# Optimization experiments

Hardware: AMD Instinct MI355X
Metric: run time of the kernel (lower is better)

The kernel has to match this reference:

```python
import jax, jax.numpy as jnp
import numpy as np

B, N, E = 8, 4096, 131072
NODE_DIM, HIDDEN = 64, 128


def _mlp2(x, W1, b1, W2, b2):
    # Linear -> SiLU -> Linear
    return jax.nn.silu(x @ W1 + b1) @ W2 + b2


def setup_inputs() -> dict:
    key = jax.random.key(0)
    ks = jax.random.split(key, 10)
    inp = {
        "node_features": jax.random.normal(ks[0], (B, N, NODE_DIM), jnp.float32),
        "coords": jax.random.normal(ks[1], (B, N, 3), jnp.float32),
        "edge_index": jax.random.randint(ks[2], (2, E), 0, N, jnp.int32),
        # message_net: in = 2*node_dim + 1 = 129
        "Wm1": jax.random.normal(ks[3], (2 * NODE_DIM + 1, HIDDEN), jnp.float32) * 0.05,
        "bm1": jnp.zeros((HIDDEN,), jnp.float32),
        "Wm2": jax.random.normal(ks[4], (HIDDEN, HIDDEN), jnp.float32) * 0.05,
        "bm2": jnp.zeros((HIDDEN,), jnp.float32),
        # node_update: in = node_dim + hidden = 192
        "Wn1": jax.random.normal(ks[5], (NODE_DIM + HIDDEN, HIDDEN), jnp.float32) * 0.05,
        "bn1": jnp.zeros((HIDDEN,), jnp.float32),
        "Wn2": jax.random.normal(ks[6], (HIDDEN, NODE_DIM), jnp.float32) * 0.05,
        "bn2": jnp.zeros((NODE_DIM,), jnp.float32),
        # coord_update: hidden -> hidden -> 1
        "Wc1": jax.random.normal(ks[7], (HIDDEN, HIDDEN), jnp.float32) * 0.05,
        "bc1": jnp.zeros((HIDDEN,), jnp.float32),
        "Wc2": jax.random.normal(ks[8], (HIDDEN, 1), jnp.float32) * 0.05,
        "bc2": jnp.zeros((1,), jnp.float32),
    }
    return inp


def reference(node_features, coords, edge_index, Wm1, bm1, Wm2, bm2,
              Wn1, bn1, Wn2, bn2, Wc1, bc1, Wc2, bc2):
    src, dst = edge_index[0], edge_index[1]
    # Gather per-edge geometry: [B, E, 3]
    edge_vec = coords[:, dst, :] - coords[:, src, :]
    edge_dist = jnp.linalg.norm(edge_vec, axis=-1, keepdims=True)  # [B,E,1]
    edge_vec_n = edge_vec / (edge_dist + 1e-8)
    # Gather node features per edge and build message input: [B, E, 2*D+1]
    msg_in = jnp.concatenate(
        [node_features[:, src, :], node_features[:, dst, :], edge_dist], axis=-1)
    messages = _mlp2(msg_in, Wm1, bm1, Wm2, bm2)  # [B, E, H]
    # Scatter-add messages into destination nodes: [B, N, H]
    agg = jnp.zeros((node_features.shape[0], node_features.shape[1], messages.shape[-1]),
                    dtype=messages.dtype).at[:, dst, :].add(messages)
    # Residual node update
    nf_new = node_features + _mlp2(
        jnp.concatenate([node_features, agg], axis=-1), Wn1, bn1, Wn2, bn2)
    # Equivariant coordinate update
    coord_w = _mlp2(messages, Wc1, bc1, Wc2, bc2)  # [B, E, 1]
    coord_delta = jnp.zeros_like(coords).at[:, dst, :].add(coord_w * edge_vec_n)
    coords_new = coords + coord_delta
    return nf_new, coords_new
```

## Files before the change

### kernel.cpp

```cpp
#include <hip/hip_runtime.h>
#include <hip/hip_bf16.h>

#define B_ 8
#define N_ 4096
#define E_ 131072
#define D_ 64
#define H_ 128

#define EDGE_BLOCKS 256
#define ETILE 128
#define TILES_TOTAL ((B_ * E_) / ETILE)
#define TILES_PER_BLOCK (TILES_TOTAL / EDGE_BLOCKS)

typedef unsigned int u32;
typedef short bf16x8 __attribute__((ext_vector_type(8)));
typedef float f32x4 __attribute__((ext_vector_type(4)));

__device__ __forceinline__ unsigned short f2bf(float f) {
  u32 x = __float_as_uint(f);
  x += 0x7fffu + ((x >> 16) & 1u);
  return (unsigned short)(x >> 16);
}
__device__ __forceinline__ float bf2f(unsigned short v) {
  return __uint_as_float(((u32)v) << 16);
}
__device__ __forceinline__ float silu_f(float x) { return x / (1.0f + __expf(-x)); }

__device__ __forceinline__ int swz(int row, int col) {
  return row * 128 + (col ^ ((row & 7) << 3));
}

__device__ __forceinline__ void gemm128(const unsigned short* in,
                                        const unsigned short* wT,
                                        int rA, int rB, int k0l, f32x4 acc[2][2]) {
#pragma unroll
  for (int ks = 0; ks < 4; ++ks) {
    const int k = ks * 32 + k0l;
    bf16x8 a0 = *(const bf16x8*)&in[swz(rA, k)];
    bf16x8 a1 = *(const bf16x8*)&in[swz(rA + 16, k)];
    bf16x8 b0 = *(const bf16x8*)&wT[swz(rB, k)];
    bf16x8 b1 = *(const bf16x8*)&wT[swz(rB + 16, k)];
    acc[0][0] = __builtin_amdgcn_mfma_f32_16x16x32_bf16(a0, b0, acc[0][0], 0, 0, 0);
    acc[0][1] = __builtin_amdgcn_mfma_f32_16x16x32_bf16(a0, b1, acc[0][1], 0, 0, 0);
    acc[1][0] = __builtin_amdgcn_mfma_f32_16x16x32_bf16(a1, b0, acc[1][0], 0, 0, 0);
    acc[1][1] = __builtin_amdgcn_mfma_f32_16x16x32_bf16(a1, b1, acc[1][1], 0, 0, 0);
  }
}

__global__ void nf2bf_k(const float* __restrict__ nf, unsigned short* __restrict__ nf16) {
  const int i = blockIdx.x * 256 + threadIdx.x;
  float4 v = ((const float4*)nf)[i];
  u32 p0 = (u32)f2bf(v.x) | ((u32)f2bf(v.y) << 16);
  u32 p1 = (u32)f2bf(v.z) | ((u32)f2bf(v.w) << 16);
  ((uint2*)nf16)[i] = make_uint2(p0, p1);
}

__global__ void hist_k(const int* __restrict__ ei, int* __restrict__ hist) {
  const int e = blockIdx.x * 256 + threadIdx.x;
  atomicAdd(&hist[ei[E_ + e]], 1);
}

__global__ __launch_bounds__(1024) void scan4096(int* __restrict__ h) {
  __shared__ int wsums[16];
  const int tid = threadIdx.x;
  const int lane = tid & 63, wv = tid >> 6;
  int4 v = ((int4*)h)[tid];
  const int s = v.x + v.y + v.z + v.w;
  int incl = s;
#pragma unroll
  for (int off = 1; off < 64; off <<= 1) {
    int u = __shfl_up(incl, off);
    if (lane >= off) incl += u;
  }
  if (lane == 63) wsums[wv] = incl;
  __syncthreads();
  if (wv == 0) {
    int ws = (lane < 16) ? wsums[lane] : 0;
#pragma unroll
    for (int off = 1; off < 16; off <<= 1) {
      int u = __shfl_up(ws, off);
      if (lane >= off) ws += u;
    }
    if (lane < 16) wsums[lane] = ws;
  }
  __syncthreads();
  int base = (wv ? wsums[wv - 1] : 0) + (incl - s);
  int4 o;
  o.x = base; o.y = base + v.x; o.z = o.y + v.y; o.w = o.z + v.z;
  ((int4*)h)[tid] = o;
}

__global__ void scatter_k(const int* __restrict__ ei, int* __restrict__ offs,
                          int* __restrict__ src_s, int* __restrict__ dst_s) {
  const int e = blockIdx.x * 256 + threadIdx.x;
  const int d = ei[E_ + e];
  const int p = atomicAdd(&offs[d], 1);
  src_s[p] = ei[e];
  dst_s[p] = d;
}

__global__ __launch_bounds__(1024, 4) void egnn_edge_mfma(
    const unsigned short* __restrict__ nf16, const float* __restrict__ coords,
    const int* __restrict__ src_s, const int* __restrict__ dst_s,
    const float* __restrict__ Wm1, const float* __restrict__ bm1,
    const float* __restrict__ Wm2, const float* __restrict__ bm2,
    const float* __restrict__ Wc1, const float* __restrict__ bc1,
    const float* __restrict__ Wc2, const float* __restrict__ bc2,
    float* __restrict__ agg, float* __restrict__ cdelta)
{
  __shared__ unsigned short sW1[128 * 128];
  __shared__ unsigned short sW2[128 * 128];
  __shared__ unsigned short sW3[128 * 128];
  __shared__ unsigned short buf[ETILE * 128];
  __shared__ float4 sgeo[2][ETILE];
  __shared__ int sdst[2][ETILE];
  __shared__ float swpart[4][ETILE];

  const int tid = threadIdx.x;
  for (int i = tid; i < 128 * 128; i += 1024) {
    const int k = i >> 7, n = i & 127;
    const int d = swz(n, k);
    sW1[d] = f2bf(Wm1[i]);
    sW2[d] = f2bf(Wm2[i]);
    sW3[d] = f2bf(Wc1[i]);
  }

  const int lane = tid & 63;
  const int w = tid >> 6;
  const int l15 = lane & 15;
  const int l4 = lane >> 4;
  const int k0l = l4 * 8;
  const int rowbase = (w >> 2) * 32;
  const int colbase = (w & 3) * 32;
  const int rA = rowbase + l15;
  const int rB = colbase + l15;
  const int n0 = colbase + l15;
  const int n1 = n0 + 16;

  const float bb1_0 = bm1[n0], bb1_1 = bm1[n1];
  const float bb2_0 = bm2[n0], bb2_1 = bm2[n1];
  const float bb3_0 = bc1[n0], bb3_1 = bc1[n1];
  const float wc2_0 = Wc2[n0], wc2_1 = Wc2[n1];
  const float wr_0 = Wm1[128 * 128 + n0], wr_1 = Wm1[128 * 128 + n1];
  const float bc2v = bc2[0];

  const int m_t = tid >> 3;
  const int q_t = tid & 7;

  const int myblk = (blockIdx.x & 7) * (EDGE_BLOCKS / 8) + (blockIdx.x >> 3);
  const int b = myblk >> 5;
  const int gbase = (myblk & 31) * TILES_PER_BLOCK;

  __syncthreads();

  for (int t = 0; t < TILES_PER_BLOCK; ++t) {
    const int p = t & 1;
    const int ebase = (gbase + t) * ETILE;

    if (tid < ETILE) {
      const int e = ebase + tid;
      const int s = src_s[e];
      const int d = dst_s[e];
      sdst[p][tid] = d;
      const float* cs = coords + (size_t)(b * N_ + s) * 3;
      const float* cd = coords + (size_t)(b * N_ + d) * 3;
      const float d0 = cd[0] - cs[0], d1 = cd[1] - cs[1], d2 = cd[2] - cs[2];
      const float dist = sqrtf(fmaf(d0, d0, fmaf(d1, d1, d2 * d2)));
      sgeo[p][tid] = make_float4(d0, d1, d2, dist);
    }
    {
      const int e = ebase + m_t;
      const int s = src_s[e];
      const int d = dst_s[e];
      const uint4* ps = (const uint4*)(nf16 + (size_t)(b * N_ + s) * 64);
      const uint4* pd = (const uint4*)(nf16 + (size_t)(b * N_ + d) * 64);
      uint4 vs = ps[q_t];
      uint4 vd = pd[q_t];
      *(uint4*)&buf[swz(m_t, q_t * 8)] = vs;
      *(uint4*)&buf[swz(m_t, 64 + q_t * 8)] = vd;
    }
    __syncthreads();

    f32x4 acc[2][2];
    {
      f32x4 z = {0.f, 0.f, 0.f, 0.f};
      acc[0][0] = z; acc[0][1] = z; acc[1][0] = z; acc[1][1] = z;
    }
    gemm128(buf, sW1, rA, rB, k0l, acc);
    float hv[2][2][4];
#pragma unroll
    for (int i = 0; i < 2; ++i)
#pragma unroll
      for (int r = 0; r < 4; ++r) {
        const int m = rowbase + 16 * i + l4 * 4 + r;
        const float dist = sgeo[p][m].w;
        hv[i][0][r] = silu_f(acc[i][0][r] + bb1_0 + dist * wr_0);
        hv[i][1][r] = silu_f(acc[i][1][r] + bb1_1 + dist * wr_1);
      }
    __syncthreads();
#pragma unroll
    for (int i = 0; i < 2; ++i)
#pragma unroll
      for (int r = 0; r < 4; ++r) {
        const int m = rowbase + 16 * i + l4 * 4 + r;
        buf[swz(m, n0)] = f2bf(hv[i][0][r]);
        buf[swz(m, n1)] = f2bf(hv[i][1][r]);
      }
    __syncthreads();

    {
      f32x4 z = {0.f, 0.f, 0.f, 0.f};
      acc[0][0] = z; acc[0][1] = z; acc[1][0] = z; acc[1][1] = z;
    }
    gemm128(buf, sW2, rA, rB, k0l, acc);
    float mv0[2][4], mv1[2][4];
#pragma unroll
    for (int i = 0; i < 2; ++i)
#pragma unroll
      for (int r = 0; r < 4; ++r) {
        mv0[i][r] = acc[i][0][r] + bb2_0;
        mv1[i][r] = acc[i][1][r] + bb2_1;
      }
    __syncthreads();
#pragma unroll
    for (int i = 0; i < 2; ++i)
#pragma unroll
      for (int r = 0; r < 4; ++r) {
        const int m = rowbase + 16 * i + l4 * 4 + r;
        buf[swz(m, n0)] = f2bf(mv0[i][r]);
        buf[swz(m, n1)] = f2bf(mv1[i][r]);
      }
    __syncthreads();

    {
      f32x4 z = {0.f, 0.f, 0.f, 0.f};
      acc[0][0] = z; acc[0][1] = z; acc[1][0] = z; acc[1][1] = z;
    }
    gemm128(buf, sW3, rA, rB, k0l, acc);
#pragma unroll
    for (int i = 0; i < 2; ++i)
#pragma unroll
      for (int r = 0; r < 4; ++r) {
        float pw = silu_f(acc[i][0][r] + bb3_0) * wc2_0 +
                   silu_f(acc[i][1][r] + bb3_1) * wc2_1;
        pw += __shfl_xor(pw, 1);
        pw += __shfl_xor(pw, 2);
        pw += __shfl_xor(pw, 4);
        pw += __shfl_xor(pw, 8);
        if (l15 == 0) swpart[w & 3][rowbase + 16 * i + l4 * 4 + r] = pw;
      }

    {
      const int c = tid & 127;
      int r = (tid >> 7) * 16;
      int cur = sdst[p][r];
      float accs = 0.f;
#pragma unroll 4
      for (int k = 0; k < 16; ++k, ++r) {
        const int d2 = sdst[p][r];
        if (d2 != cur) {
          unsafeAtomicAdd(agg + ((size_t)(b * N_ + cur)) * H_ + c, accs);
          accs = 0.f;
          cur = d2;
        }
        accs += bf2f(buf[swz(r, c)]);
      }
      unsafeAtomicAdd(agg + ((size_t)(b * N_ + cur)) * H_ + c, accs);
    }
    __syncthreads();

    if (tid < ETILE) {
      float wc = bc2v;
#pragma unroll
      for (int cg = 0; cg < 4; ++cg) wc += swpart[cg][tid];
      const float4 g = sgeo[p][tid];
      const float inv = 1.0f / (g.w + 1e-8f);
      float vx = wc * g.x * inv, vy = wc * g.y * inv, vz = wc * g.z * inv;
      const int myd = sdst[p][tid];
      int flg = (lane == 0) ? 1 : (sdst[p][tid - 1] != myd);
#pragma unroll
      for (int off = 1; off < 64; off <<= 1) {
        float ux = __shfl_up(vx, off);
        float uy = __shfl_up(vy, off);
        float uz = __shfl_up(vz, off);
        int uf = __shfl_up(flg, off);
        if (lane >= off) {
          if (!flg) { vx += ux; vy += uy; vz += uz; }
          flg |= uf;
        }
      }
      const bool tail = (lane == 63) || (sdst[p][tid + 1] != myd);
      if (tail) {
        float* bp = cdelta + ((size_t)(b * N_ + myd)) * 3;
        unsafeAtomicAdd(bp + 0, vx);
        unsafeAtomicAdd(bp + 1, vy);
        unsafeAtomicAdd(bp + 2, vz);
      }
    }
  }
}

__device__ __forceinline__ float bfbits(u32 x) { return __uint_as_float(x); }

__global__ __launch_bounds__(512, 2) void egnn_node(
    const float* __restrict__ nf, const float* __restrict__ coords,
    const float* __restrict__ agg, const float* __restrict__ cdelta,
    const float* __restrict__ Wn1, const float* __restrict__ bn1,
    const float* __restrict__ Wn2, const float* __restrict__ bn2,
    float* __restrict__ out_nf, float* __restrict__ out_c)
{
  __shared__ unsigned short sWn1[192 * H_];
  __shared__ unsigned short sWn2[H_ * D_];
  __shared__ float sb[192];
  __shared__ float swork[8][328];

  const int tid = threadIdx.x;
  for (int i = tid; i < 192 * H_; i += 512) sWn1[i] = f2bf(Wn1[i]);
  for (int i = tid; i < H_ * D_; i += 512) sWn2[i] = f2bf(Wn2[i]);
  if (tid < 128) sb[tid] = bn1[tid];
  if (tid >= 128 && tid < 192) sb[tid] = bn2[tid - 128];
  __syncthreads();

  const int wave = tid >> 6;
  const int lane = tid & 63;
  float* W = swork[wave];

  const int total = B_ * N_;
  const int stride = gridDim.x * 8;

  for (int task = blockIdx.x * 8 + wave; task < total; task += stride) {
    const float* nfp = nf + (size_t)task * D_;
    const float* ap = agg + (size_t)task * H_;
    W[lane] = nfp[lane];
    W[64 + lane] = ap[lane];
    W[128 + lane] = ap[64 + lane];
    __syncthreads();

    {
      const unsigned short* wp = sWn1 + 2 * lane;
      float a0 = 0.f, a1 = 0.f, a2 = 0.f, a3 = 0.f;
#pragma unroll 8
      for (int k = 0; k < 192; k += 2) {
        float2 x = *(const float2*)&W[k];
        u32 p0 = *(const u32*)(wp + k * H_);
        u32 p1 = *(const u32*)(wp + (k + 1) * H_);
        a0 = fmaf(x.x, bfbits(p0 << 16), a0);
        a1 = fmaf(x.x, bfbits(p0 & 0xffff0000u), a1);
        a2 = fmaf(x.y, bfbits(p1 << 16), a2);
        a3 = fmaf(x.y, bfbits(p1 & 0xffff0000u), a3);
      }
      float h0 = silu_f(a0 + a2 + sb[2 * lane]);
      float h1 = silu_f(a1 + a3 + sb[2 * lane + 1]);
      ((float2*)(W + 192))[lane] = make_float2(h0, h1);
    }
    __syncthreads();

    {
      float a0 = 0.f, a1 = 0.f, a2 = 0.f, a3 = 0.f;
#pragma unroll 8
      for (int k = 0; k < 128; k += 4) {
        float2 xa = *(const float2*)&W[192 + k];
        float2 xb = *(const float2*)&W[192 + k + 2];
        a0 = fmaf(xa.x, bfbits(((u32)sWn2[(k + 0) * D_ + lane]) << 16), a0);
        a1 = fmaf(xa.y, bfbits(((u32)sWn2[(k + 1) * D_ + lane]) << 16), a1);
        a2 = fmaf(xb.x, bfbits(((u32)sWn2[(k + 2) * D_ + lane]) << 16), a2);
        a3 = fmaf(xb.y, bfbits(((u32)sWn2[(k + 3) * D_ + lane]) << 16), a3);
      }
      out_nf[(size_t)task * D_ + lane] =
          nfp[lane] + (a0 + a1 + a2 + a3) + sb[128 + lane];
      if (lane < 3) {
        out_c[(size_t)task * 3 + lane] =
            coords[(size_t)task * 3 + lane] + cdelta[(size_t)task * 3 + lane];
      }
    }
    __syncthreads();
  }
}

extern "C" void kernel_launch(void* const* d_in, const int* in_sizes, int n_in,
                              void* d_out, int out_size, void* d_ws, size_t ws_size,
                              hipStream_t stream) {
  const float* nf     = (const float*)d_in[0];
  const float* coords = (const float*)d_in[1];
  const int*   ei     = (const int*)d_in[2];
  const float* Wm1 = (const float*)d_in[3];
  const float* bm1 = (const float*)d_in[4];
  const float* Wm2 = (const float*)d_in[5];
  const float* bm2 = (const float*)d_in[6];
  const float* Wn1 = (const float*)d_in[7];
  const float* bn1 = (const float*)d_in[8];
  const float* Wn2 = (const float*)d_in[9];
  const float* bn2 = (const float*)d_in[10];
  const float* Wc1 = (const float*)d_in[11];
  const float* bc1 = (const float*)d_in[12];
  const float* Wc2 = (const float*)d_in[13];
  const float* bc2 = (const float*)d_in[14];

  float* agg    = (float*)d_ws;
  float* cdelta = agg + (size_t)B_ * N_ * H_;
  int*   hist   = (int*)(cdelta + (size_t)B_ * N_ * 3);
  int*   src_s  = hist + 4096;
  int*   dst_s  = src_s + E_;

  float* out_nf = (float*)d_out;
  float* out_c  = out_nf + (size_t)B_ * N_ * D_;

  unsigned short* nf16 = (unsigned short*)d_out;

  const size_t zero_bytes =
      ((size_t)B_ * N_ * H_ + (size_t)B_ * N_ * 3 + 4096) * sizeof(float);
  hipMemsetAsync(d_ws, 0, zero_bytes, stream);

  nf2bf_k<<<(B_ * N_ * D_ / 4) / 256, 256, 0, stream>>>(nf, nf16);
  hist_k<<<E_ / 256, 256, 0, stream>>>(ei, hist);
  scan4096<<<1, 1024, 0, stream>>>(hist);
  scatter_k<<<E_ / 256, 256, 0, stream>>>(ei, hist, src_s, dst_s);

  egnn_edge_mfma<<<EDGE_BLOCKS, 1024, 0, stream>>>(
      nf16, coords, src_s, dst_s, Wm1, bm1, Wm2, bm2, Wc1, bc1, Wc2, bc2,
      agg, cdelta);
  egnn_node<<<512, 512, 0, stream>>>(nf, coords, agg, cdelta,
                                     Wn1, bn1, Wn2, bn2, out_nf, out_c);
}
```

Before: 456.0 us.

## Double edge tile, register-resident Wc1 fragments, prefetch next tile gathers

Doubles the edge tile to 256 rows so each wave computes a 64x32 output block, reusing each B fragment across four A fragments. The third weight matrix is held in registers instead of LDS, which frees shared memory for the larger buffer. Node-feature gathers and geometry for the next tile are prefetched into registers and the spare sgeo/sdst buffer while the current tile computes. Float-to-bf16 conversion now uses the packed hardware instruction. The cost is much higher register pressure under launch_bounds(1024,4), which risks spills or lower occupancy.

```diff
diff --git a/kernel.cpp b/kernel.cpp
--- a/kernel.cpp
+++ b/kernel.cpp
@@ -8,7 +8,7 @@
 #define H_ 128
 
 #define EDGE_BLOCKS 256
-#define ETILE 128
+#define ETILE 256
 #define TILES_TOTAL ((B_ * E_) / ETILE)
 #define TILES_PER_BLOCK (TILES_TOTAL / EDGE_BLOCKS)
 
@@ -24,34 +24,24 @@
 __device__ __forceinline__ float bf2f(unsigned short v) {
   return __uint_as_float(((u32)v) << 16);
 }
+__device__ __forceinline__ u32 cvt_pk_bf16(float lo, float hi) {
+  u32 r;
+  asm("v_cvt_pk_bf16_f32 %0, %1, %2" : "=v"(r) : "v"(lo), "v"(hi));
+  return r;
+}
 __device__ __forceinline__ float silu_f(float x) { return x / (1.0f + __expf(-x)); }
 
 __device__ __forceinline__ int swz(int row, int col) {
   return row * 128 + (col ^ ((row & 7) << 3));
 }
 
-__device__ __forceinline__ void gemm128(const unsigned short* in,
-                                        const unsigned short* wT,
-                                        int rA, int rB, int k0l, f32x4 acc[2][2]) {
-#pragma unroll
-  for (int ks = 0; ks < 4; ++ks) {
-    const int k = ks * 32 + k0l;
-    bf16x8 a0 = *(const bf16x8*)&in[swz(rA, k)];
-    bf16x8 a1 = *(const bf16x8*)&in[swz(rA + 16, k)];
-    bf16x8 b0 = *(const bf16x8*)&wT[swz(rB, k)];
-    bf16x8 b1 = *(const bf16x8*)&wT[swz(rB + 16, k)];
-    acc[0][0] = __builtin_amdgcn_mfma_f32_16x16x32_bf16(a0, b0, acc[0][0], 0, 0, 0);
-    acc[0][1] = __builtin_amdgcn_mfma_f32_16x16x32_bf16(a0, b1, acc[0][1], 0, 0, 0);
-    acc[1][0] = __builtin_amdgcn_mfma_f32_16x16x32_bf16(a1, b0, acc[1][0], 0, 0, 0);
-    acc[1][1] = __builtin_amdgcn_mfma_f32_16x16x32_bf16(a1, b1, acc[1][1], 0, 0, 0);
-  }
-}
+#define MFMA(a, b, c) __builtin_amdgcn_mfma_f32_16x16x32_bf16(a, b, c, 0, 0, 0)
 
 __global__ void nf2bf_k(const float* __restrict__ nf, unsigned short* __restrict__ nf16) {
   const int i = blockIdx.x * 256 + threadIdx.x;
   float4 v = ((const float4*)nf)[i];
-  u32 p0 = (u32)f2bf(v.x) | ((u32)f2bf(v.y) << 16);
-  u32 p1 = (u32)f2bf(v.z) | ((u32)f2bf(v.w) << 16);
+  u32 p0 = cvt_pk_bf16(v.x, v.y);
+  u32 p1 = cvt_pk_bf16(v.z, v.w);
   ((uint2*)nf16)[i] = make_uint2(p0, p1);
 }
 
@@ -110,7 +100,6 @@
 {
   __shared__ unsigned short sW1[128 * 128];
   __shared__ unsigned short sW2[128 * 128];
-  __shared__ unsigned short sW3[128 * 128];
   __shared__ unsigned short buf[ETILE * 128];
   __shared__ float4 sgeo[2][ETILE];
   __shared__ int sdst[2][ETILE];
@@ -122,7 +111,6 @@
     const int d = swz(n, k);
     sW1[d] = f2bf(Wm1[i]);
     sW2[d] = f2bf(Wm2[i]);
-    sW3[d] = f2bf(Wc1[i]);
   }
 
   const int lane = tid & 63;
@@ -130,10 +118,8 @@
   const int l15 = lane & 15;
   const int l4 = lane >> 4;
   const int k0l = l4 * 8;
-  const int rowbase = (w >> 2) * 32;
+  const int rowbase = (w >> 2) * 64;
   const int colbase = (w & 3) * 32;
-  const int rA = rowbase + l15;
-  const int rB = colbase + l15;
   const int n0 = colbase + l15;
   const int n1 = n0 + 16;
 
@@ -144,78 +130,140 @@
   const float wr_0 = Wm1[128 * 128 + n0], wr_1 = Wm1[128 * 128 + n1];
   const float bc2v = bc2[0];
 
-  const int m_t = tid >> 3;
-  const int q_t = tid & 7;
+  bf16x8 w3f[2][4];
+#pragma unroll
+  for (int cb = 0; cb < 2; ++cb) {
+    const int n = colbase + cb * 16 + l15;
+#pragma unroll
+    for (int ks = 0; ks < 4; ++ks) {
+      bf16x8 v;
+#pragma unroll
+      for (int j = 0; j < 8; ++j)
+        v[j] = (short)f2bf(Wc1[(ks * 32 + k0l + j) * 128 + n]);
+      w3f[cb][ks] = v;
+    }
+  }
 
   const int myblk = (blockIdx.x & 7) * (EDGE_BLOCKS / 8) + (blockIdx.x >> 3);
   const int b = myblk >> 5;
   const int gbase = (myblk & 31) * TILES_PER_BLOCK;
 
-  __syncthreads();
-
-  for (int t = 0; t < TILES_PER_BLOCK; ++t) {
-    const int p = t & 1;
-    const int ebase = (gbase + t) * ETILE;
-
+  const int m_p = tid >> 2;
+  const int q_p = tid & 3;
+
+  {
+    const int ebase0 = gbase * ETILE;
     if (tid < ETILE) {
-      const int e = ebase + tid;
+      const int e = ebase0 + tid;
       const int s = src_s[e];
       const int d = dst_s[e];
-      sdst[p][tid] = d;
+      sdst[0][tid] = d;
       const float* cs = coords + (size_t)(b * N_ + s) * 3;
       const float* cd = coords + (size_t)(b * N_ + d) * 3;
       const float d0 = cd[0] - cs[0], d1 = cd[1] - cs[1], d2 = cd[2] - cs[2];
       const float dist = sqrtf(fmaf(d0, d0, fmaf(d1, d1, d2 * d2)));
-      sgeo[p][tid] = make_float4(d0, d1, d2, dist);
-    }
-    {
-      const int e = ebase + m_t;
-      const int s = src_s[e];
-      const int d = dst_s[e];
-      const uint4* ps = (const uint4*)(nf16 + (size_t)(b * N_ + s) * 64);
-      const uint4* pd = (const uint4*)(nf16 + (size_t)(b * N_ + d) * 64);
-      uint4 vs = ps[q_t];
-      uint4 vd = pd[q_t];
-      *(uint4*)&buf[swz(m_t, q_t * 8)] = vs;
-      *(uint4*)&buf[swz(m_t, 64 + q_t * 8)] = vd;
-    }
-    __syncthreads();
-
-    f32x4 acc[2][2];
+      sgeo[0][tid] = make_float4(d0, d1, d2, dist);
+    }
+  }
+  uint4 pf[4];
+  {
+    const int e = gbase * ETILE + m_p;
+    const int node = (q_p < 2) ? src_s[e] : dst_s[e];
+    const unsigned short* np = nf16 + (size_t)(b * N_ + node) * 64 + (q_p & 1) * 32;
+#pragma unroll
+    for (int j = 0; j < 4; ++j) pf[j] = *(const uint4*)(np + j * 8);
+  }
+
+  f32x4 acc[4][2];
+
+  for (int t = 0; t < TILES_PER_BLOCK; ++t) {
+    const int p = t & 1;
+
+#pragma unroll
+    for (int j = 0; j < 4; ++j)
+      *(uint4*)&buf[swz(m_p, (q_p * 4 + j) * 8)] = pf[j];
+    __syncthreads();
+
+    {
+      const int tt = (t + 1 < TILES_PER_BLOCK) ? t + 1 : t;
+      const int ebase2 = (gbase + tt) * ETILE;
+      const int e = ebase2 + m_p;
+      const int node = (q_p < 2) ? src_s[e] : dst_s[e];
+      const unsigned short* np = nf16 + (size_t)(b * N_ + node) * 64 + (q_p & 1) * 32;
+#pragma unroll
+      for (int j = 0; j < 4; ++j) pf[j] = *(const uint4*)(np + j * 8);
+      if (tid < ETILE) {
+        const int e2 = ebase2 + tid;
+        const int s = src_s[e2];
+        const int d = dst_s[e2];
+        sdst[p ^ 1][tid] = d;
+        const float* cs = coords + (size_t)(b * N_ + s) * 3;
+        const float* cd = coords + (size_t)(b * N_ + d) * 3;
+        const float d0 = cd[0] - cs[0], d1 = cd[1] - cs[1], d2 = cd[2] - cs[2];
+        const float dist = sqrtf(fmaf(d0, d0, fmaf(d1, d1, d2 * d2)));
+        sgeo[p ^ 1][tid] = make_float4(d0, d1, d2, dist);
+      }
+    }
+
     {
       f32x4 z = {0.f, 0.f, 0.f, 0.f};
-      acc[0][0] = z; acc[0][1] = z; acc[1][0] = z; acc[1][1] = z;
-    }
-    gemm128(buf, sW1, rA, rB, k0l, acc);
-    float hv[2][2][4];
-#pragma unroll
-    for (int i = 0; i < 2; ++i)
+#pragma unroll
+      for (int i = 0; i < 4; ++i) { acc[i][0] = z; acc[i][1] = z; }
+    }
+#pragma unroll
+    for (int ks = 0; ks < 4; ++ks) {
+      const int k = ks * 32 + k0l;
+      bf16x8 b0 = *(const bf16x8*)&sW1[swz(colbase + l15, k)];
+      bf16x8 b1 = *(const bf16x8*)&sW1[swz(colbase + 16 + l15, k)];
+#pragma unroll
+      for (int i = 0; i < 4; ++i) {
+        bf16x8 a = *(const bf16x8*)&buf[swz(rowbase + 16 * i + l15, k)];
+        acc[i][0] = MFMA(a, b0, acc[i][0]);
+        acc[i][1] = MFMA(a, b1, acc[i][1]);
+      }
+    }
+    float hv0[4][4], hv1[4][4];
+#pragma unroll
+    for (int i = 0; i < 4; ++i)
 #pragma unroll
       for (int r = 0; r < 4; ++r) {
         const int m = rowbase + 16 * i + l4 * 4 + r;
         const float dist = sgeo[p][m].w;
-        hv[i][0][r] = silu_f(acc[i][0][r] + bb1_0 + dist * wr_0);
-        hv[i][1][r] = silu_f(acc[i][1][r] + bb1_1 + dist * wr_1);
-      }
-    __syncthreads();
-#pragma unroll
-    for (int i = 0; i < 2; ++i)
+        hv0[i][r] = silu_f(acc[i][0][r] + bb1_0 + dist * wr_0);
+        hv1[i][r] = silu_f(acc[i][1][r] + bb1_1 + dist * wr_1);
+      }
+    __syncthreads();
+#pragma unroll
+    for (int i = 0; i < 4; ++i)
 #pragma unroll
       for (int r = 0; r < 4; ++r) {
         const int m = rowbase + 16 * i + l4 * 4 + r;
-        buf[swz(m, n0)] = f2bf(hv[i][0][r]);
-        buf[swz(m, n1)] = f2bf(hv[i][1][r]);
+        const u32 pk = cvt_pk_bf16(hv0[i][r], hv1[i][r]);
+        buf[swz(m, n0)] = (unsigned short)pk;
+        buf[swz(m, n1)] = (unsigned short)(pk >> 16);
       }
     __syncthreads();
 
     {
       f32x4 z = {0.f, 0.f, 0.f, 0.f};
-      acc[0][0] = z; acc[0][1] = z; acc[1][0] = z; acc[1][1] = z;
-    }
-    gemm128(buf, sW2, rA, rB, k0l, acc);
-    float mv0[2][4], mv1[2][4];
-#pragma unroll
-    for (int i = 0; i < 2; ++i)
+#pragma unroll
+      for (int i = 0; i < 4; ++i) { acc[i][0] = z; acc[i][1] = z; }
+    }
+#pragma unroll
+    for (int ks = 0; ks < 4; ++ks) {
+      const int k = ks * 32 + k0l;
+      bf16x8 b0 = *(const bf16x8*)&sW2[swz(colbase + l15, k)];
+      bf16x8 b1 = *(const bf16x8*)&sW2[swz(colbase + 16 + l15, k)];
+#pragma unroll
+      for (int i = 0; i < 4; ++i) {
+        bf16x8 a = *(const bf16x8*)&buf[swz(rowbase + 16 * i + l15, k)];
+        acc[i][0] = MFMA(a, b0, acc[i][0]);
+        acc[i][1] = MFMA(a, b1, acc[i][1]);
+      }
+    }
+    float mv0[4][4], mv1[4][4];
+#pragma unroll
+    for (int i = 0; i < 4; ++i)
 #pragma unroll
       for (int r = 0; r < 4; ++r) {
         mv0[i][r] = acc[i][0][r] + bb2_0;
@@ -223,22 +271,33 @@
       }
     __syncthreads();
 #pragma unroll
-    for (int i = 0; i < 2; ++i)
+    for (int i = 0; i < 4; ++i)
 #pragma unroll
       for (int r = 0; r < 4; ++r) {
         const int m = rowbase + 16 * i + l4 * 4 + r;
-        buf[swz(m, n0)] = f2bf(mv0[i][r]);
-        buf[swz(m, n1)] = f2bf(mv1[i][r]);
+        const u32 pk = cvt_pk_bf16(mv0[i][r], mv1[i][r]);
+        buf[swz(m, n0)] = (unsigned short)pk;
+        buf[swz(m, n1)] = (unsigned short)(pk >> 16);
       }
     __syncthreads();
 
     {
       f32x4 z = {0.f, 0.f, 0.f, 0.f};
-      acc[0][0] = z; acc[0][1] = z; acc[1][0] = z; acc[1][1] = z;
-    }
-    gemm128(buf, sW3, rA, rB, k0l, acc);
-#pragma unroll
-    for (int i = 0; i < 2; ++i)
+#pragma unroll
+      for (int i = 0; i < 4; ++i) { acc[i][0] = z; acc[i][1] = z; }
+    }
+#pragma unroll
+    for (int ks = 0; ks < 4; ++ks) {
+      const int k = ks * 32 + k0l;
+#pragma unroll
+      for (int i = 0; i < 4; ++i) {
+        bf16x8 a = *(const bf16x8*)&buf[swz(rowbase + 16 * i + l15, k)];
+        acc[i][0] = MFMA(a, w3f[0][ks], acc[i][0]);
+        acc[i][1] = MFMA(a, w3f[1][ks], acc[i][1]);
+      }
+    }
+#pragma unroll
+    for (int i = 0; i < 4; ++i)
 #pragma unroll
       for (int r = 0; r < 4; ++r) {
         float pw = silu_f(acc[i][0][r] + bb3_0) * wc2_0 +
@@ -252,11 +311,11 @@
 
     {
       const int c = tid & 127;
-      int r = (tid >> 7) * 16;
+      int r = (tid >> 7) * 32;
       int cur = sdst[p][r];
       float accs = 0.f;
 #pragma unroll 4
-      for (int k = 0; k < 16; ++k, ++r) {
+      for (int k = 0; k < 32; ++k, ++r) {
         const int d2 = sdst[p][r];
         if (d2 != cur) {
           unsafeAtomicAdd(agg + ((size_t)(b * N_ + cur)) * H_ + c, accs);
```

Result: slower. 541.1 us (+18.7%).

## Ping-pong LDS activation buffers, keep Wc1 in registers, use packed bf16 converts

Applied to the files above, without the earlier changes.

Replaces the single shared activation buffer with two ping-pong buffers (bufA/bufB), so each layer writes its output directly into the other buffer. This removes the extra __syncthreads between reading the accumulators and writing the next layer's inputs. The third weight matrix (Wc1) moves from LDS into per-thread register fragments, which frees the LDS it used. Float-to-bf16 conversion now uses the hardware v_cvt_pk_bf16_f32 instruction, and the occupancy hint in launch_bounds is dropped. The register-resident weights raise VGPR pressure and could reduce occupancy or cause spills.

```diff
diff --git a/kernel.cpp b/kernel.cpp
--- a/kernel.cpp
+++ b/kernel.cpp
@@ -24,34 +24,24 @@
 __device__ __forceinline__ float bf2f(unsigned short v) {
   return __uint_as_float(((u32)v) << 16);
 }
+__device__ __forceinline__ u32 cvt_pk_bf16(float lo, float hi) {
+  u32 r;
+  asm("v_cvt_pk_bf16_f32 %0, %1, %2" : "=v"(r) : "v"(lo), "v"(hi));
+  return r;
+}
 __device__ __forceinline__ float silu_f(float x) { return x / (1.0f + __expf(-x)); }
 
 __device__ __forceinline__ int swz(int row, int col) {
   return row * 128 + (col ^ ((row & 7) << 3));
 }
 
-__device__ __forceinline__ void gemm128(const unsigned short* in,
-                                        const unsigned short* wT,
-                                        int rA, int rB, int k0l, f32x4 acc[2][2]) {
-#pragma unroll
-  for (int ks = 0; ks < 4; ++ks) {
-    const int k = ks * 32 + k0l;
-    bf16x8 a0 = *(const bf16x8*)&in[swz(rA, k)];
-    bf16x8 a1 = *(const bf16x8*)&in[swz(rA + 16, k)];
-    bf16x8 b0 = *(const bf16x8*)&wT[swz(rB, k)];
-    bf16x8 b1 = *(const bf16x8*)&wT[swz(rB + 16, k)];
-    acc[0][0] = __builtin_amdgcn_mfma_f32_16x16x32_bf16(a0, b0, acc[0][0], 0, 0, 0);
-    acc[0][1] = __builtin_amdgcn_mfma_f32_16x16x32_bf16(a0, b1, acc[0][1], 0, 0, 0);
-    acc[1][0] = __builtin_amdgcn_mfma_f32_16x16x32_bf16(a1, b0, acc[1][0], 0, 0, 0);
-    acc[1][1] = __builtin_amdgcn_mfma_f32_16x16x32_bf16(a1, b1, acc[1][1], 0, 0, 0);
-  }
-}
+#define MFMA(a, b, c) __builtin_amdgcn_mfma_f32_16x16x32_bf16(a, b, c, 0, 0, 0)
 
 __global__ void nf2bf_k(const float* __restrict__ nf, unsigned short* __restrict__ nf16) {
   const int i = blockIdx.x * 256 + threadIdx.x;
   float4 v = ((const float4*)nf)[i];
-  u32 p0 = (u32)f2bf(v.x) | ((u32)f2bf(v.y) << 16);
-  u32 p1 = (u32)f2bf(v.z) | ((u32)f2bf(v.w) << 16);
+  u32 p0 = cvt_pk_bf16(v.x, v.y);
+  u32 p1 = cvt_pk_bf16(v.z, v.w);
   ((uint2*)nf16)[i] = make_uint2(p0, p1);
 }
 
@@ -99,7 +89,7 @@
   dst_s[p] = d;
 }
 
-__global__ __launch_bounds__(1024, 4) void egnn_edge_mfma(
+__global__ __launch_bounds__(1024) void egnn_edge_mfma(
     const unsigned short* __restrict__ nf16, const float* __restrict__ coords,
     const int* __restrict__ src_s, const int* __restrict__ dst_s,
     const float* __restrict__ Wm1, const float* __restrict__ bm1,
@@ -110,8 +100,8 @@
 {
   __shared__ unsigned short sW1[128 * 128];
   __shared__ unsigned short sW2[128 * 128];
-  __shared__ unsigned short sW3[128 * 128];
-  __shared__ unsigned short buf[ETILE * 128];
+  __shared__ unsigned short bufA[ETILE * 128];
+  __shared__ unsigned short bufB[ETILE * 128];
   __shared__ float4 sgeo[2][ETILE];
   __shared__ int sdst[2][ETILE];
   __shared__ float swpart[4][ETILE];
@@ -122,7 +112,6 @@
     const int d = swz(n, k);
     sW1[d] = f2bf(Wm1[i]);
     sW2[d] = f2bf(Wm2[i]);
-    sW3[d] = f2bf(Wc1[i]);
   }
 
   const int lane = tid & 63;
@@ -132,8 +121,6 @@
   const int k0l = l4 * 8;
   const int rowbase = (w >> 2) * 32;
   const int colbase = (w & 3) * 32;
-  const int rA = rowbase + l15;
-  const int rB = colbase + l15;
   const int n0 = colbase + l15;
   const int n1 = n0 + 16;
 
@@ -144,14 +131,30 @@
   const float wr_0 = Wm1[128 * 128 + n0], wr_1 = Wm1[128 * 128 + n1];
   const float bc2v = bc2[0];
 
-  const int m_t = tid >> 3;
-  const int q_t = tid & 7;
+  bf16x8 w3f[2][4];
+#pragma unroll
+  for (int cb = 0; cb < 2; ++cb) {
+    const int n = colbase + cb * 16 + l15;
+#pragma unroll
+    for (int ks = 0; ks < 4; ++ks) {
+      bf16x8 v;
+#pragma unroll
+      for (int j = 0; j < 8; ++j)
+        v[j] = (short)f2bf(Wc1[(ks * 32 + k0l + j) * 128 + n]);
+      w3f[cb][ks] = v;
+    }
+  }
 
   const int myblk = (blockIdx.x & 7) * (EDGE_BLOCKS / 8) + (blockIdx.x >> 3);
   const int b = myblk >> 5;
   const int gbase = (myblk & 31) * TILES_PER_BLOCK;
 
+  const int m_t = tid >> 3;
+  const int q_t = tid & 7;
+
   __syncthreads();
+
+  f32x4 acc[2][2];
 
   for (int t = 0; t < TILES_PER_BLOCK; ++t) {
     const int p = t & 1;
@@ -176,35 +179,65 @@
       const uint4* pd = (const uint4*)(nf16 + (size_t)(b * N_ + d) * 64);
       uint4 vs = ps[q_t];
       uint4 vd = pd[q_t];
-      *(uint4*)&buf[swz(m_t, q_t * 8)] = vs;
-      *(uint4*)&buf[swz(m_t, 64 + q_t * 8)] = vd;
-    }
-    __syncthreads();
-
-    f32x4 acc[2][2];
+      *(uint4*)&bufA[swz(m_t, q_t * 8)] = vs;
+      *(uint4*)&bufA[swz(m_t, 64 + q_t * 8)] = vd;
+    }
+    __syncthreads();
+
     {
       f32x4 z = {0.f, 0.f, 0.f, 0.f};
       acc[0][0] = z; acc[0][1] = z; acc[1][0] = z; acc[1][1] = z;
     }
-    gemm128(buf, sW1, rA, rB, k0l, acc);
-    float hv[2][2][4];
+#pragma unroll
+    for (int ks = 0; ks < 4; ++ks) {
+      const int k = ks * 32 + k0l;
+      bf16x8 b0 = *(const bf16x8*)&sW1[swz(colbase + l15, k)];
+      bf16x8 b1 = *(const bf16x8*)&sW1[swz(colbase + 16 + l15, k)];
+      bf16x8 a0 = *(const bf16x8*)&bufA[swz(rowbase + l15, k)];
+      bf16x8 a1 = *(const bf16x8*)&bufA[swz(rowbase + 16 + l15, k)];
+      acc[0][0] = MFMA(a0, b0, acc[0][0]);
+      acc[0][1] = MFMA(a0, b1, acc[0][1]);
+      acc[1][0] = MFMA(a1, b0, acc[1][0]);
+      acc[1][1] = MFMA(a1, b1, acc[1][1]);
+    }
 #pragma unroll
     for (int i = 0; i < 2; ++i)
 #pragma unroll
       for (int r = 0; r < 4; ++r) {
         const int m = rowbase + 16 * i + l4 * 4 + r;
         const float dist = sgeo[p][m].w;
-        hv[i][0][r] = silu_f(acc[i][0][r] + bb1_0 + dist * wr_0);
-        hv[i][1][r] = silu_f(acc[i][1][r] + bb1_1 + dist * wr_1);
-      }
-    __syncthreads();
+        const float h0 = silu_f(acc[i][0][r] + bb1_0 + dist * wr_0);
+        const float h1 = silu_f(acc[i][1][r] + bb1_1 + dist * wr_1);
+        const u32 pk = cvt_pk_bf16(h0, h1);
+        bufB[swz(m, n0)] = (unsigned short)pk;
+        bufB[swz(m, n1)] = (unsigned short)(pk >> 16);
+      }
+    __syncthreads();
+
+    {
+      f32x4 z = {0.f, 0.f, 0.f, 0.f};
+      acc[0][0] = z; acc[0][1] = z; acc[1][0] = z; acc[1][1] = z;
+    }
+#pragma unroll
+    for (int ks = 0; ks < 4; ++ks) {
+      const int k = ks * 32 + k0l;
+      bf16x8 b0 = *(const bf16x8*)&sW2[swz(colbase + l15, k)];
+      bf16x8 b1 = *(const bf16x8*)&sW2[swz(colbase + 16 + l15, k)];
+      bf16x8 a0 = *(const bf16x8*)&bufB[swz(rowbase + l15, k)];
+      bf16x8 a1 = *(const bf16x8*)&bufB[swz(rowbase + 16 + l15, k)];
+      acc[0][0] = MFMA(a0, b0, acc[0][0]);
+      acc[0][1] = MFMA(a0, b1, acc[0][1]);
+      acc[1][0] = MFMA(a1, b0, acc[1][0]);
+      acc[1][1] = MFMA(a1, b1, acc[1][1]);
+    }
 #pragma unroll
     for (int i = 0; i < 2; ++i)
 #pragma unroll
       for (int r = 0; r < 4; ++r) {
         const int m = rowbase + 16 * i + l4 * 4 + r;
-        buf[swz(m, n0)] = f2bf(hv[i][0][r]);
-        buf[swz(m, n1)] = f2bf(hv[i][1][r]);
+        const u32 pk = cvt_pk_bf16(acc[i][0][r] + bb2_0, acc[i][1][r] + bb2_1);
+        bufA[swz(m, n0)] = (unsigned short)pk;
+        bufA[swz(m, n1)] = (unsigned short)(pk >> 16);
       }
     __syncthreads();
 
@@ -212,31 +245,16 @@
       f32x4 z = {0.f, 0.f, 0.f, 0.f};
       acc[0][0] = z; acc[0][1] = z; acc[1][0] = z; acc[1][1] = z;
     }
-    gemm128(buf, sW2, rA, rB, k0l, acc);
-    float mv0[2][4], mv1[2][4];
-#pragma unroll
-    for (int i = 0; i < 2; ++i)
-#pragma unroll
-      for (int r = 0; r < 4; ++r) {
-        mv0[i][r] = acc[i][0][r] + bb2_0;
-        mv1[i][r] = acc[i][1][r] + bb2_1;
-      }
-    __syncthreads();
-#pragma unroll
-    for (int i = 0; i < 2; ++i)
-#pragma unroll
-      for (int r = 0; r < 4; ++r) {
-        const int m = rowbase + 16 * i + l4 * 4 + r;
-        buf[swz(m, n0)] = f2bf(mv0[i][r]);
-        buf[swz(m, n1)] = f2bf(mv1[i][r]);
-      }
-    __syncthreads();
-
-    {
-      f32x4 z = {0.f, 0.f, 0.f, 0.f};
-      acc[0][0] = z; acc[0][1] = z; acc[1][0] = z; acc[1][1] = z;
-    }
-    gemm128(buf, sW3, rA, rB, k0l, acc);
+#pragma unroll
+    for (int ks = 0; ks < 4; ++ks) {
+      const int k = ks * 32 + k0l;
+      bf16x8 a0 = *(const bf16x8*)&bufA[swz(rowbase + l15, k)];
+      bf16x8 a1 = *(const bf16x8*)&bufA[swz(rowbase + 16 + l15, k)];
+      acc[0][0] = MFMA(a0, w3f[0][ks], acc[0][0]);
+      acc[0][1] = MFMA(a0, w3f[1][ks], acc[0][1]);
+      acc[1][0] = MFMA(a1, w3f[0][ks], acc[1][0]);
+      acc[1][1] = MFMA(a1, w3f[1][ks], acc[1][1]);
+    }
 #pragma unroll
     for (int i = 0; i < 2; ++i)
 #pragma unroll
@@ -263,7 +281,7 @@
           accs = 0.f;
           cur = d2;
         }
-        accs += bf2f(buf[swz(r, c)]);
+        accs += bf2f(bufA[swz(r, c)]);
       }
       unsafeAtomicAdd(agg + ((size_t)(b * N_ + cur)) * H_ + c, accs);
     }
```

After: 542.1 us. 18.9% more time.

## Rewrite node-update MLP as tiled bf16 MFMA kernel and use packed bf16 convert

Applied to the files above, without the earlier changes.

Replaces the per-node scalar FMA node-update kernel with a 128-node tile kernel that stages bf16 node features, aggregates and swizzled transposed weights in LDS and computes both MLP layers with MFMA. It also replaces the manual bf16 rounding in the conversion kernel with the hardware packed convert instruction, and inlines the edge GEMM helper with B loads issued before A loads. Each block reconverts the weights, and the large LDS footprint limits residency.

```diff
diff --git a/kernel.cpp b/kernel.cpp
--- a/kernel.cpp
+++ b/kernel.cpp
@@ -24,34 +24,24 @@
 __device__ __forceinline__ float bf2f(unsigned short v) {
   return __uint_as_float(((u32)v) << 16);
 }
+__device__ __forceinline__ u32 cvt_pk_bf16(float lo, float hi) {
+  u32 r;
+  asm("v_cvt_pk_bf16_f32 %0, %1, %2" : "=v"(r) : "v"(lo), "v"(hi));
+  return r;
+}
 __device__ __forceinline__ float silu_f(float x) { return x / (1.0f + __expf(-x)); }
 
 __device__ __forceinline__ int swz(int row, int col) {
   return row * 128 + (col ^ ((row & 7) << 3));
 }
 
-__device__ __forceinline__ void gemm128(const unsigned short* in,
-                                        const unsigned short* wT,
-                                        int rA, int rB, int k0l, f32x4 acc[2][2]) {
-#pragma unroll
-  for (int ks = 0; ks < 4; ++ks) {
-    const int k = ks * 32 + k0l;
-    bf16x8 a0 = *(const bf16x8*)&in[swz(rA, k)];
-    bf16x8 a1 = *(const bf16x8*)&in[swz(rA + 16, k)];
-    bf16x8 b0 = *(const bf16x8*)&wT[swz(rB, k)];
-    bf16x8 b1 = *(const bf16x8*)&wT[swz(rB + 16, k)];
-    acc[0][0] = __builtin_amdgcn_mfma_f32_16x16x32_bf16(a0, b0, acc[0][0], 0, 0, 0);
-    acc[0][1] = __builtin_amdgcn_mfma_f32_16x16x32_bf16(a0, b1, acc[0][1], 0, 0, 0);
-    acc[1][0] = __builtin_amdgcn_mfma_f32_16x16x32_bf16(a1, b0, acc[1][0], 0, 0, 0);
-    acc[1][1] = __builtin_amdgcn_mfma_f32_16x16x32_bf16(a1, b1, acc[1][1], 0, 0, 0);
-  }
-}
+#define MFMA(a, b, c) __builtin_amdgcn_mfma_f32_16x16x32_bf16(a, b, c, 0, 0, 0)
 
 __global__ void nf2bf_k(const float* __restrict__ nf, unsigned short* __restrict__ nf16) {
   const int i = blockIdx.x * 256 + threadIdx.x;
   float4 v = ((const float4*)nf)[i];
-  u32 p0 = (u32)f2bf(v.x) | ((u32)f2bf(v.y) << 16);
-  u32 p1 = (u32)f2bf(v.z) | ((u32)f2bf(v.w) << 16);
+  u32 p0 = cvt_pk_bf16(v.x, v.y);
+  u32 p1 = cvt_pk_bf16(v.z, v.w);
   ((uint2*)nf16)[i] = make_uint2(p0, p1);
 }
 
@@ -186,7 +176,18 @@
       f32x4 z = {0.f, 0.f, 0.f, 0.f};
       acc[0][0] = z; acc[0][1] = z; acc[1][0] = z; acc[1][1] = z;
     }
-    gemm128(buf, sW1, rA, rB, k0l, acc);
+#pragma unroll
+    for (int ks = 0; ks < 4; ++ks) {
+      const int k = ks * 32 + k0l;
+      bf16x8 b0 = *(const bf16x8*)&sW1[swz(rB, k)];
+      bf16x8 b1 = *(const bf16x8*)&sW1[swz(rB + 16, k)];
+      bf16x8 a0 = *(const bf16x8*)&buf[swz(rA, k)];
+      bf16x8 a1 = *(const bf16x8*)&buf[swz(rA + 16, k)];
+      acc[0][0] = MFMA(a0, b0, acc[0][0]);
+      acc[0][1] = MFMA(a0, b1, acc[0][1]);
+      acc[1][0] = MFMA(a1, b0, acc[1][0]);
+      acc[1][1] = MFMA(a1, b1, acc[1][1]);
+    }
     float hv[2][2][4];
 #pragma unroll
     for (int i = 0; i < 2; ++i)
@@ -212,7 +213,18 @@
       f32x4 z = {0.f, 0.f, 0.f, 0.f};
       acc[0][0] = z; acc[0][1] = z; acc[1][0] = z; acc[1][1] = z;
     }
-    gemm128(buf, sW2, rA, rB, k0l, acc);
+#pragma unroll
+    for (int ks = 0; ks < 4; ++ks) {
+      const int k = ks * 32 + k0l;
+      bf16x8 b0 = *(const bf16x8*)&sW2[swz(rB, k)];
+      bf16x8 b1 = *(const bf16x8*)&sW2[swz(rB + 16, k)];
+      bf16x8 a0 = *(const bf16x8*)&buf[swz(rA, k)];
+      bf16x8 a1 = *(const bf16x8*)&buf[swz(rA + 16, k)];
+      acc[0][0] = MFMA(a0, b0, acc[0][0]);
+      acc[0][1] = MFMA(a0, b1, acc[0][1]);
+      acc[1][0] = MFMA(a1, b0, acc[1][0]);
+      acc[1][1] = MFMA(a1, b1, acc[1][1]);
+    }
     float mv0[2][4], mv1[2][4];
 #pragma unroll
     for (int i = 0; i < 2; ++i)
@@ -236,7 +248,18 @@
       f32x4 z = {0.f, 0.f, 0.f, 0.f};
       acc[0][0] = z; acc[0][1] = z; acc[1][0] = z; acc[1][1] = z;
     }
-    gemm128(buf, sW3, rA, rB, k0l, acc);
+#pragma unroll
+    for (int ks = 0; ks < 4; ++ks) {
+      const int k = ks * 32 + k0l;
+      bf16x8 b0 = *(const bf16x8*)&sW3[swz(rB, k)];
+      bf16x8 b1 = *(const bf16x8*)&sW3[swz(rB + 16, k)];
+      bf16x8 a0 = *(const bf16x8*)&buf[swz(rA, k)];
+      bf16x8 a1 = *(const bf16x8*)&buf[swz(rA + 16, k)];
+      acc[0][0] = MFMA(a0, b0, acc[0][0]);
+      acc[0][1] = MFMA(a0, b1, acc[0][1]);
+      acc[1][0] = MFMA(a1, b0, acc[1][0]);
+      acc[1][1] = MFMA(a1, b1, acc[1][1]);
+    }
 #pragma unroll
     for (int i = 0; i < 2; ++i)
 #pragma unroll
@@ -300,81 +323,138 @@
   }
 }
 
-__device__ __forceinline__ float bfbits(u32 x) { return __uint_as_float(x); }
-
-__global__ __launch_bounds__(512, 2) void egnn_node(
+#define NTILE 128
+
+__global__ __launch_bounds__(512) void egnn_node_mfma(
     const float* __restrict__ nf, const float* __restrict__ coords,
     const float* __restrict__ agg, const float* __restrict__ cdelta,
     const float* __restrict__ Wn1, const float* __restrict__ bn1,
     const float* __restrict__ Wn2, const float* __restrict__ bn2,
     float* __restrict__ out_nf, float* __restrict__ out_c)
 {
-  __shared__ unsigned short sWn1[192 * H_];
-  __shared__ unsigned short sWn2[H_ * D_];
-  __shared__ float sb[192];
-  __shared__ float swork[8][328];
+  __shared__ unsigned short sA[128 * 192];
+  __shared__ unsigned short sB[64 * 128];
+  __shared__ unsigned short bufN[128 * 64];
+  __shared__ unsigned short bufA[128 * 128];
+  __shared__ unsigned short hbuf[128 * 128];
 
   const int tid = threadIdx.x;
-  for (int i = tid; i < 192 * H_; i += 512) sWn1[i] = f2bf(Wn1[i]);
-  for (int i = tid; i < H_ * D_; i += 512) sWn2[i] = f2bf(Wn2[i]);
-  if (tid < 128) sb[tid] = bn1[tid];
-  if (tid >= 128 && tid < 192) sb[tid] = bn2[tid - 128];
+  const int node0 = blockIdx.x * NTILE;
+
+  for (int i = tid; i < 192 * 128; i += 512) {
+    const int k = i >> 7, n = i & 127;
+    sA[n * 192 + (k ^ ((n & 7) << 3))] = f2bf(Wn1[i]);
+  }
+  for (int i = tid; i < 128 * 64; i += 512) {
+    const int k = i >> 6, n = i & 63;
+    sB[n * 128 + (k ^ ((n & 7) << 3))] = f2bf(Wn2[i]);
+  }
+#pragma unroll
+  for (int j = 0; j < 8; ++j) {
+    const int p = tid + j * 512;
+    const int row = p >> 5, col = 2 * (p & 31);
+    float2 v = *(const float2*)&nf[(size_t)(node0 + row) * 64 + col];
+    *(u32*)&bufN[row * 64 + (col ^ ((row & 7) << 3))] = cvt_pk_bf16(v.x, v.y);
+  }
+#pragma unroll
+  for (int j = 0; j < 16; ++j) {
+    const int p = tid + j * 512;
+    const int row = p >> 6, col = 2 * (p & 63);
+    float2 v = *(const float2*)&agg[(size_t)(node0 + row) * 128 + col];
+    *(u32*)&bufA[row * 128 + (col ^ ((row & 7) << 3))] = cvt_pk_bf16(v.x, v.y);
+  }
+  if (tid < 3 * NTILE) {
+    out_c[(size_t)node0 * 3 + tid] =
+        coords[(size_t)node0 * 3 + tid] + cdelta[(size_t)node0 * 3 + tid];
+  }
+
+  const int lane = tid & 63;
+  const int w = tid >> 6;
+  const int l15 = lane & 15;
+  const int l4 = lane >> 4;
+  const int k0l = l4 * 8;
+
+  const int rb1 = (w & 1) * 64;
+  const int cb1 = (w >> 1) * 32;
+  const int n0 = cb1 + l15, n1 = n0 + 16;
+  const float bb1_0 = bn1[n0], bb1_1 = bn1[n1];
+
+  const int rb2 = (w >> 1) * 32;
+  const int cb2 = (w & 1) * 32;
+  const int n20 = cb2 + l15, n21 = n20 + 16;
+  const float bb2_0 = bn2[n20], bb2_1 = bn2[n21];
+
   __syncthreads();
 
-  const int wave = tid >> 6;
-  const int lane = tid & 63;
-  float* W = swork[wave];
-
-  const int total = B_ * N_;
-  const int stride = gridDim.x * 8;
-
-  for (int task = blockIdx.x * 8 + wave; task < total; task += stride) {
-    const float* nfp = nf + (size_t)task * D_;
-    const float* ap = agg + (size_t)task * H_;
-    W[lane] = nfp[lane];
-    W[64 + lane] = ap[lane];
-    W[128 + lane] = ap[64 + lane];
-    __syncthreads();
-
-    {
-      const unsigned short* wp = sWn1 + 2 * lane;
-      float a0 = 0.f, a1 = 0.f, a2 = 0.f, a3 = 0.f;
-#pragma unroll 8
-      for (int k = 0; k < 192; k += 2) {
-        float2 x = *(const float2*)&W[k];
-        u32 p0 = *(const u32*)(wp + k * H_);
-        u32 p1 = *(const u32*)(wp + (k + 1) * H_);
-        a0 = fmaf(x.x, bfbits(p0 << 16), a0);
-        a1 = fmaf(x.x, bfbits(p0 & 0xffff0000u), a1);
-        a2 = fmaf(x.y, bfbits(p1 << 16), a2);
-        a3 = fmaf(x.y, bfbits(p1 & 0xffff0000u), a3);
-      }
-      float h0 = silu_f(a0 + a2 + sb[2 * lane]);
-      float h1 = silu_f(a1 + a3 + sb[2 * lane + 1]);
-      ((float2*)(W + 192))[lane] = make_float2(h0, h1);
-    }
-    __syncthreads();
-
-    {
-      float a0 = 0.f, a1 = 0.f, a2 = 0.f, a3 = 0.f;
-#pragma unroll 8
-      for (int k = 0; k < 128; k += 4) {
-        float2 xa = *(const float2*)&W[192 + k];
-        float2 xb = *(const float2*)&W[192 + k + 2];
-        a0 = fmaf(xa.x, bfbits(((u32)sWn2[(k + 0) * D_ + lane]) << 16), a0);
-        a1 = fmaf(xa.y, bfbits(((u32)sWn2[(k + 1) * D_ + lane]) << 16), a1);
-        a2 = fmaf(xb.x, bfbits(((u32)sWn2[(k + 2) * D_ + lane]) << 16), a2);
-        a3 = fmaf(xb.y, bfbits(((u32)sWn2[(k + 3) * D_ + lane]) << 16), a3);
-      }
-      out_nf[(size_t)task * D_ + lane] =
-          nfp[lane] + (a0 + a1 + a2 + a3) + sb[128 + lane];
-      if (lane < 3) {
-        out_c[(size_t)task * 3 + lane] =
-            coords[(size_t)task * 3 + lane] + cdelta[(size_t)task * 3 + lane];
-      }
-    }
-    __syncthreads();
-  }
+  f32x4 acc[4][2];
+  {
+    f32x4 z = {0.f, 0.f, 0.f, 0.f};
+#pragma unroll
+    for (int i = 0; i < 4; ++i) { acc[i][0] = z; acc[i][1] = z; }
+  }
+#pragma unroll
+  for (int ks = 0; ks < 2; ++ks) {
+    const int k = ks * 32 + k0l;
+    bf16x8 b0 = *(const bf16x8*)&sA[n0 * 192 + (k ^ ((n0 & 7) << 3))];
+    bf16x8 b1 = *(const bf16x8*)&sA[n1 * 192 + (k ^ ((n1 & 7) << 3))];
+#pragma unroll
+    for (int i = 0; i < 4; ++i) {
+      const int row = rb1 + 16 * i + l15;
+      bf16x8 a = *(const bf16x8*)&bufN[row * 64 + (k ^ ((row & 7) << 3))];
+      acc[i][0] = MFMA(a, b0, acc[i][0]);
+      acc[i][1] = MFMA(a, b1, acc[i][1]);
+    }
+  }
+#pragma unroll
+  for (int ks = 0; ks < 4; ++ks) {
+    const int k = ks * 32 + k0l;
+    const int kg = 64 + k;
+    bf16x8 b0 = *(const bf16x8*)&sA[n0 * 192 + (kg ^ ((n0 & 7) << 3))];
+    bf16x8 b1 = *(const bf16x8*)&sA[n1 * 192 + (kg ^ ((n1 & 7) << 3))];
+#pragma unroll
+    for (int i = 0; i < 4; ++i) {
+      const int row = rb1 + 16 * i + l15;
+      bf16x8 a = *(const bf16x8*)&bufA[row * 128 + (k ^ ((row & 7) << 3))];
+      acc[i][0] = MFMA(a, b0, acc[i][0]);
+      acc[i][1] = MFMA(a, b1, acc[i][1]);
+    }
+  }
+#pragma unroll
+  for (int i = 0; i < 4; ++i)
+#pragma unroll
+    for (int r = 0; r < 4; ++r) {
+      const int m = rb1 + 16 * i + l4 * 4 + r;
+      hbuf[m * 128 + (n0 ^ ((m & 7) << 3))] = f2bf(silu_f(acc[i][0][r] + bb1_0));
+      hbuf[m * 128 + (n1 ^ ((m & 7) << 3))] = f2bf(silu_f(acc[i][1][r] + bb1_1));
+    }
+  __syncthreads();
+
+  {
+    f32x4 z = {0.f, 0.f, 0.f, 0.f};
+    acc[0][0] = z; acc[0][1] = z; acc[1][0] = z; acc[1][1] = z;
+  }
+#pragma unroll
+  for (int ks = 0; ks < 4; ++ks) {
+    const int k = ks * 32 + k0l;
+    bf16x8 b0 = *(const bf16x8*)&sB[n20 * 128 + (k ^ ((n20 & 7) << 3))];
+    bf16x8 b1 = *(const bf16x8*)&sB[n21 * 128 + (k ^ ((n21 & 7) << 3))];
+    const int r0 = rb2 + l15, r1 = rb2 + 16 + l15;
+    bf16x8 a0 = *(const bf16x8*)&hbuf[r0 * 128 + (k ^ ((r0 & 7) << 3))];
+    bf16x8 a1 = *(const bf16x8*)&hbuf[r1 * 128 + (k ^ ((r1 & 7) << 3))];
+    acc[0][0] = MFMA(a0, b0, acc[0][0]);
+    acc[0][1] = MFMA(a0, b1, acc[0][1]);
+    acc[1][0] = MFMA(a1, b0, acc[1][0]);
+    acc[1][1] = MFMA(a1, b1, acc[1][1]);
+  }
+#pragma unroll
+  for (int i = 0; i < 2; ++i)
+#pragma unroll
+    for (int r = 0; r < 4; ++r) {
+      const int m = rb2 + 16 * i + l4 * 4 + r;
+      const size_t base = (size_t)(node0 + m) * 64;
+      out_nf[base + n20] = nf[base + n20] + acc[i][0][r] + bb2_0;
+      out_nf[base + n21] = nf[base + n21] + acc[i][1][r] + bb2_1;
+    }
 }
 
 extern "C" void kernel_launch(void* const* d_in, const int* in_sizes, int n_in,
@@ -419,6 +499,6 @@
   egnn_edge_mfma<<<EDGE_BLOCKS, 1024, 0, stream>>>(
       nf16, coords, src_s, dst_s, Wm1, bm1, Wm2, bm2, Wc1, bc1, Wc2, bc2,
       agg, cdelta);
-  egnn_node<<<512, 512, 0, stream>>>(nf, coords, agg, cdelta,
-                                     Wn1, bn1, Wn2, bn2, out_nf, out_c);
-}
+  egnn_node_mfma<<<(B_ * N_) / NTILE, 512, 0, stream>>>(
+      nf, coords, agg, cdelta, Wn1, bn1, Wn2, bn2, out_nf, out_c);
+}
```

Measured after the change: 392.5 us. -13.9%, faster.
